# Optimization experiments

Measured on AMD Instinct MI355X. Metric: run time of the kernel, lower is better.

Reference implementation:

```python
import jax, jax.numpy as jnp
import numpy as np

B, N, IN_DIM, OUT_DIM = 8, 2048, 128, 64
TEMPERATURE = 1.0
NEG_SLOPE = 0.2


def setup_inputs() -> dict:
    key = jax.random.key(0)
    k1, k2, k3, k4, k5 = jax.random.split(key, 5)
    s_fc = 1.0 / np.sqrt(IN_DIM)
    s_at = 1.0 / np.sqrt(2 * OUT_DIM)
    return {
        "h": jax.random.normal(k1, (B, N, IN_DIM), dtype=jnp.float32),
        "W_fc": jax.random.normal(k2, (IN_DIM, OUT_DIM), dtype=jnp.float32) * s_fc,
        "b_fc": jax.random.normal(k3, (OUT_DIM,), dtype=jnp.float32) * s_fc,
        "a_src": jax.random.normal(k4, (OUT_DIM,), dtype=jnp.float32) * s_at,
        "a_dst": jax.random.normal(k5, (OUT_DIM,), dtype=jnp.float32) * s_at,
        "b_attn": jnp.zeros((), dtype=jnp.float32),
    }


def reference(h, W_fc, b_fc, a_src, a_dst, b_attn):
    # hp: (B, N, OUT_DIM) -- projected node features
    hp = h @ W_fc + b_fc
    # attn_fc(concat(h_i, h_j)) == h_i@a_src + h_j@a_dst + b (exact decomposition)
    s = hp @ a_src  # (B, N) source contribution
    d = hp @ a_dst  # (B, N) dest contribution
    scores = s[:, :, None] + d[:, None, :] + b_attn  # (B, N, N)
    scores = jnp.where(scores >= 0, scores, NEG_SLOPE * scores)  # leaky_relu
    scores = scores / TEMPERATURE
    attn = jax.nn.softmax(scores, axis=-1)
    out = jnp.einsum("bij,bjd->bid", attn, hp)
    return jax.nn.elu(out)
```

## Files before the change

### kernel.cpp

```cpp
#include <hip/hip_runtime.h>
#include <hip/hip_bf16.h>
#include <math.h>

#define BB 8
#define NN 2048
#define IND 128
#define OUTD 64
#define NEG 0.2f

typedef __attribute__((ext_vector_type(8))) short short8;
typedef __attribute__((ext_vector_type(4))) float f32x4;

__device__ __forceinline__ unsigned short f2bf(float f) {
    unsigned int u = __float_as_uint(f);
    u += 0x7fffu + ((u >> 16) & 1u);
    return (unsigned short)(u >> 16);
}

__device__ __forceinline__ unsigned int pk_bf16(float a, float b) {
    union { __hip_bfloat162 h; unsigned int u; } cv;
    cv.h = __float22bfloat162_rn(make_float2(a, b));
    return cv.u;
}

__global__ __launch_bounds__(256) void gat_proj_kernel(
    const float* __restrict__ h, const float* __restrict__ W,
    const float* __restrict__ bfc, const float* __restrict__ asrc,
    const float* __restrict__ adst,
    unsigned short* __restrict__ hpT2, float* __restrict__ s,
    float* __restrict__ F, float* __restrict__ H)
{
    __shared__ float Wl[IND * OUTD];
    __shared__ float hl[32 * 132];

    const int t  = threadIdx.x;
    const int R0 = blockIdx.x * 32;

    const float4* W4 = (const float4*)W;
    float4*       Wl4 = (float4*)Wl;
    #pragma unroll
    for (int k2 = 0; k2 < 8; ++k2) Wl4[t + k2 * 256] = W4[t + k2 * 256];

    const float4* h4 = (const float4*)(h + (size_t)R0 * IND);
    #pragma unroll
    for (int k2 = 0; k2 < 4; ++k2) {
        const int idx = t + k2 * 256;
        const int row = idx >> 5, c4 = idx & 31;
        *(float4*)&hl[row * 132 + c4 * 4] = h4[idx];
    }
    __syncthreads();

    const int r0 = (t >> 4) * 2;
    const int o0 = (t & 15) * 4;
    const float4 bias = *(const float4*)(bfc + o0);
    float4 a0 = bias, a1 = bias;

    #pragma unroll 2
    for (int kc = 0; kc < IND; kc += 4) {
        const float4 w0 = *(const float4*)&Wl[(kc + 0) * OUTD + o0];
        const float4 w1 = *(const float4*)&Wl[(kc + 1) * OUTD + o0];
        const float4 w2 = *(const float4*)&Wl[(kc + 2) * OUTD + o0];
        const float4 w3 = *(const float4*)&Wl[(kc + 3) * OUTD + o0];
        const float4 h0 = *(const float4*)&hl[(r0 + 0) * 132 + kc];
        const float4 h1 = *(const float4*)&hl[(r0 + 1) * 132 + kc];

        a0.x = fmaf(h0.x, w0.x, a0.x); a0.y = fmaf(h0.x, w0.y, a0.y);
        a0.z = fmaf(h0.x, w0.z, a0.z); a0.w = fmaf(h0.x, w0.w, a0.w);
        a0.x = fmaf(h0.y, w1.x, a0.x); a0.y = fmaf(h0.y, w1.y, a0.y);
        a0.z = fmaf(h0.y, w1.z, a0.z); a0.w = fmaf(h0.y, w1.w, a0.w);
        a0.x = fmaf(h0.z, w2.x, a0.x); a0.y = fmaf(h0.z, w2.y, a0.y);
        a0.z = fmaf(h0.z, w2.z, a0.z); a0.w = fmaf(h0.z, w2.w, a0.w);
        a0.x = fmaf(h0.w, w3.x, a0.x); a0.y = fmaf(h0.w, w3.y, a0.y);
        a0.z = fmaf(h0.w, w3.z, a0.z); a0.w = fmaf(h0.w, w3.w, a0.w);

        a1.x = fmaf(h1.x, w0.x, a1.x); a1.y = fmaf(h1.x, w0.y, a1.y);
        a1.z = fmaf(h1.x, w0.z, a1.z); a1.w = fmaf(h1.x, w0.w, a1.w);
        a1.x = fmaf(h1.y, w1.x, a1.x); a1.y = fmaf(h1.y, w1.y, a1.y);
        a1.z = fmaf(h1.y, w1.z, a1.z); a1.w = fmaf(h1.y, w1.w, a1.w);
        a1.x = fmaf(h1.z, w2.x, a1.x); a1.y = fmaf(h1.z, w2.y, a1.y);
        a1.z = fmaf(h1.z, w2.z, a1.z); a1.w = fmaf(h1.z, w2.w, a1.w);
        a1.x = fmaf(h1.w, w3.x, a1.x); a1.y = fmaf(h1.w, w3.y, a1.y);
        a1.z = fmaf(h1.w, w3.z, a1.z); a1.w = fmaf(h1.w, w3.w, a1.w);
    }

    const int b   = R0 >> 11;
    const int jb0 = (R0 & 2047) + r0;
    const int cj  = jb0 >> 3;
    const int sub = jb0 & 7;
    unsigned short* cbase = hpT2 + (((size_t)(b * 256 + cj)) * OUTD) * 8;
    {
        ushort2 v;
        v.x = f2bf(a0.x); v.y = f2bf(a1.x);
        *(ushort2*)(cbase + (o0 + 0) * 8 + sub) = v;
        v.x = f2bf(a0.y); v.y = f2bf(a1.y);
        *(ushort2*)(cbase + (o0 + 1) * 8 + sub) = v;
        v.x = f2bf(a0.z); v.y = f2bf(a1.z);
        *(ushort2*)(cbase + (o0 + 2) * 8 + sub) = v;
        v.x = f2bf(a0.w); v.y = f2bf(a1.w);
        *(ushort2*)(cbase + (o0 + 3) * 8 + sub) = v;
    }

    const float4 as4 = *(const float4*)(asrc + o0);
    const float4 ad4 = *(const float4*)(adst + o0);
    float vs[2], vd[2];
    vs[0] = a0.x*as4.x + a0.y*as4.y + a0.z*as4.z + a0.w*as4.w;
    vs[1] = a1.x*as4.x + a1.y*as4.y + a1.z*as4.z + a1.w*as4.w;
    vd[0] = a0.x*ad4.x + a0.y*ad4.y + a0.z*ad4.z + a0.w*ad4.w;
    vd[1] = a1.x*ad4.x + a1.y*ad4.y + a1.z*ad4.z + a1.w*ad4.w;
    #pragma unroll
    for (int msk = 1; msk <= 8; msk <<= 1) {
        vs[0] += __shfl_xor(vs[0], msk);
        vs[1] += __shfl_xor(vs[1], msk);
        vd[0] += __shfl_xor(vd[0], msk);
        vd[1] += __shfl_xor(vd[1], msk);
    }
    if ((t & 15) == 0) {
        #pragma unroll
        for (int r = 0; r < 2; ++r) {
            s[R0 + r0 + r] = vs[r];
            F[R0 + r0 + r] = __expf(vd[r]);
            H[R0 + r0 + r] = __expf(NEG * vd[r]);
        }
    }
}

__global__ __launch_bounds__(256) void gat_attn_kernel(
    const unsigned short* __restrict__ hpT2, const float* __restrict__ s,
    const float* __restrict__ F, const float* __restrict__ H,
    const float* __restrict__ battn_p, float* __restrict__ out)
{
    __shared__ float accl[4][64 * 66];
    __shared__ float ll[4][64];

    const int t    = threadIdx.x;
    const int lane = t & 63;
    const int wv   = t >> 6;
    const int blk  = blockIdx.x;
    const int b    = blk >> 5;
    const int i0   = (blk & 31) * 64;
    const int m    = lane & 15;
    const int kc   = lane >> 4;

    const float battn = battn_p[0];
    float E[4], G[4];
    #pragma unroll
    for (int T = 0; T < 4; ++T) {
        const float smv = s[b * NN + i0 + T * 16 + m] + battn;
        E[T] = __expf(smv);
        G[T] = __expf(NEG * smv);
    }
    const float* Fb = F + b * NN;
    const float* Hb = H + b * NN;
    const unsigned short* hb = hpT2 + (size_t)b * 256 * OUTD * 8;

    short8 ones;
    #pragma unroll
    for (int q = 0; q < 8; ++q) ones[q] = (short)0x3F80;

    f32x4 acc[4][4];
    f32x4 dacc[4];
    #pragma unroll
    for (int T = 0; T < 4; ++T) {
        dacc[T] = (f32x4){0.f, 0.f, 0.f, 0.f};
        #pragma unroll
        for (int ot = 0; ot < 4; ++ot) acc[T][ot] = (f32x4){0.f, 0.f, 0.f, 0.f};
    }

    const int jbase = wv * (NN / 4);

    #pragma unroll 2
    for (int it = 0; it < NN / 4 / 32; ++it) {
        const int j0 = jbase + it * 32;
        const size_t cb = ((size_t)((j0 >> 3) + kc)) * OUTD * 8;
        const short8 bf0 = *(const short8*)(hb + cb + (0 * 16 + m) * 8);
        const short8 bf1 = *(const short8*)(hb + cb + (1 * 16 + m) * 8);
        const short8 bf2 = *(const short8*)(hb + cb + (2 * 16 + m) * 8);
        const short8 bf3 = *(const short8*)(hb + cb + (3 * 16 + m) * 8);

        const float4 Fa = *(const float4*)(Fb + j0 + kc * 8);
        const float4 Fc = *(const float4*)(Fb + j0 + kc * 8 + 4);
        const float4 Ha = *(const float4*)(Hb + j0 + kc * 8);
        const float4 Hc = *(const float4*)(Hb + j0 + kc * 8 + 4);

        #pragma unroll
        for (int T = 0; T < 4; ++T) {
            const float Ei = E[T], Gi = G[T];
            float wf[8];
            wf[0] = fmaxf(Ei * Fa.x, Gi * Ha.x);
            wf[1] = fmaxf(Ei * Fa.y, Gi * Ha.y);
            wf[2] = fmaxf(Ei * Fa.z, Gi * Ha.z);
            wf[3] = fmaxf(Ei * Fa.w, Gi * Ha.w);
            wf[4] = fmaxf(Ei * Fc.x, Gi * Hc.x);
            wf[5] = fmaxf(Ei * Fc.y, Gi * Hc.y);
            wf[6] = fmaxf(Ei * Fc.z, Gi * Hc.z);
            wf[7] = fmaxf(Ei * Fc.w, Gi * Hc.w);

            union { short8 s8; unsigned int u[4]; } af;
            af.u[0] = pk_bf16(wf[0], wf[1]);
            af.u[1] = pk_bf16(wf[2], wf[3]);
            af.u[2] = pk_bf16(wf[4], wf[5]);
            af.u[3] = pk_bf16(wf[6], wf[7]);

            acc[T][0] = __builtin_amdgcn_mfma_f32_16x16x32_bf16(af.s8, bf0, acc[T][0], 0, 0, 0);
            acc[T][1] = __builtin_amdgcn_mfma_f32_16x16x32_bf16(af.s8, bf1, acc[T][1], 0, 0, 0);
            acc[T][2] = __builtin_amdgcn_mfma_f32_16x16x32_bf16(af.s8, bf2, acc[T][2], 0, 0, 0);
            acc[T][3] = __builtin_amdgcn_mfma_f32_16x16x32_bf16(af.s8, bf3, acc[T][3], 0, 0, 0);
            dacc[T]   = __builtin_amdgcn_mfma_f32_16x16x32_bf16(af.s8, ones, dacc[T], 0, 0, 0);
        }
    }

    if (m == 0) {
        #pragma unroll
        for (int T = 0; T < 4; ++T)
            #pragma unroll
            for (int r = 0; r < 4; ++r) ll[wv][T * 16 + kc * 4 + r] = dacc[T][r];
    }

    #pragma unroll
    for (int T = 0; T < 4; ++T) {
        #pragma unroll
        for (int r = 0; r < 4; ++r) {
            const int row = T * 16 + kc * 4 + r;
            accl[wv][row * 66 + 0 * 16 + m] = acc[T][0][r];
            accl[wv][row * 66 + 1 * 16 + m] = acc[T][1][r];
            accl[wv][row * 66 + 2 * 16 + m] = acc[T][2][r];
            accl[wv][row * 66 + 3 * 16 + m] = acc[T][3][r];
        }
    }
    __syncthreads();

    const int col = t & 63;
    const int r0e = (t >> 6) * 16;
    float* ob = out + (((size_t)b * NN + i0) * OUTD);
    #pragma unroll 4
    for (int r = 0; r < 16; ++r) {
        const int row = r0e + r;
        const float lsum = (ll[0][row] + ll[1][row]) + (ll[2][row] + ll[3][row]);
        float v = (accl[0][row * 66 + col] + accl[1][row * 66 + col]) +
                  (accl[2][row * 66 + col] + accl[3][row * 66 + col]);
        v /= lsum;
        v = (v > 0.f) ? v : expm1f(v);
        ob[(size_t)row * OUTD + col] = v;
    }
}

extern "C" void kernel_launch(void* const* d_in, const int* in_sizes, int n_in,
                              void* d_out, int out_size, void* d_ws, size_t ws_size,
                              hipStream_t stream)
{
    const float* h     = (const float*)d_in[0];
    const float* W     = (const float*)d_in[1];
    const float* bfc   = (const float*)d_in[2];
    const float* asrc  = (const float*)d_in[3];
    const float* adst  = (const float*)d_in[4];
    const float* battn = (const float*)d_in[5];
    float* out = (float*)d_out;

    unsigned short* hpT2 = (unsigned short*)d_ws;
    float* s = (float*)((char*)d_ws + (size_t)BB * NN * OUTD * 2);
    float* F = s + (size_t)BB * NN;
    float* H = F + (size_t)BB * NN;

    gat_proj_kernel<<<(BB * NN) / 32, 256, 0, stream>>>(h, W, bfc, asrc, adst,
                                                        hpT2, s, F, H);
    gat_attn_kernel<<<BB * (NN / 64), 256, 0, stream>>>(hpT2, s, F, H, battn, out);
}
```

Baseline: 91.17 us.

## Switch attention path to fp16 packed math and eight-wave blocks

Projected features and the exp factors F/H are stored as fp16 instead of bf16/fp32. Attention weights are built with packed half2 multiply/max instead of scalar fp32 ops plus bf16 conversion, and fed to f16 MFMA. Both kernels move to 512-thread blocks: the attention kernel splits the j range over eight waves and reduces partial accumulators through shared memory in two phases. This cuts VALU work and load bandwidth in the inner loop, at the cost of fp16 range risk for exp values and an extra sync in the reduction.

```diff
diff --git a/kernel.cpp b/kernel.cpp
--- a/kernel.cpp
+++ b/kernel.cpp
@@ -1,5 +1,4 @@
 #include <hip/hip_runtime.h>
-#include <hip/hip_bf16.h>
 #include <math.h>
 
 #define BB 8
@@ -8,43 +7,38 @@
 #define OUTD 64
 #define NEG 0.2f
 
-typedef __attribute__((ext_vector_type(8))) short short8;
 typedef __attribute__((ext_vector_type(4))) float f32x4;
-
-__device__ __forceinline__ unsigned short f2bf(float f) {
-    unsigned int u = __float_as_uint(f);
-    u += 0x7fffu + ((u >> 16) & 1u);
-    return (unsigned short)(u >> 16);
-}
-
-__device__ __forceinline__ unsigned int pk_bf16(float a, float b) {
-    union { __hip_bfloat162 h; unsigned int u; } cv;
-    cv.h = __float22bfloat162_rn(make_float2(a, b));
-    return cv.u;
-}
-
-__global__ __launch_bounds__(256) void gat_proj_kernel(
+typedef __attribute__((ext_vector_type(2))) _Float16 h2;
+typedef __attribute__((ext_vector_type(8))) _Float16 half8;
+
+__device__ __forceinline__ unsigned short f2h(float f) {
+    union { _Float16 h; unsigned short u; } c;
+    c.h = (_Float16)f;
+    return c.u;
+}
+
+__global__ __launch_bounds__(512) void gat_proj_kernel(
     const float* __restrict__ h, const float* __restrict__ W,
     const float* __restrict__ bfc, const float* __restrict__ asrc,
     const float* __restrict__ adst,
     unsigned short* __restrict__ hpT2, float* __restrict__ s,
-    float* __restrict__ F, float* __restrict__ H)
+    _Float16* __restrict__ F, _Float16* __restrict__ H)
 {
     __shared__ float Wl[IND * OUTD];
-    __shared__ float hl[32 * 132];
+    __shared__ float hl[64 * 132];
 
     const int t  = threadIdx.x;
-    const int R0 = blockIdx.x * 32;
+    const int R0 = blockIdx.x * 64;
 
     const float4* W4 = (const float4*)W;
     float4*       Wl4 = (float4*)Wl;
     #pragma unroll
-    for (int k2 = 0; k2 < 8; ++k2) Wl4[t + k2 * 256] = W4[t + k2 * 256];
+    for (int k2 = 0; k2 < 4; ++k2) Wl4[t + k2 * 512] = W4[t + k2 * 512];
 
     const float4* h4 = (const float4*)(h + (size_t)R0 * IND);
     #pragma unroll
     for (int k2 = 0; k2 < 4; ++k2) {
-        const int idx = t + k2 * 256;
+        const int idx = t + k2 * 512;
         const int row = idx >> 5, c4 = idx & 31;
         *(float4*)&hl[row * 132 + c4 * 4] = h4[idx];
     }
@@ -90,13 +84,13 @@
     unsigned short* cbase = hpT2 + (((size_t)(b * 256 + cj)) * OUTD) * 8;
     {
         ushort2 v;
-        v.x = f2bf(a0.x); v.y = f2bf(a1.x);
+        v.x = f2h(a0.x); v.y = f2h(a1.x);
         *(ushort2*)(cbase + (o0 + 0) * 8 + sub) = v;
-        v.x = f2bf(a0.y); v.y = f2bf(a1.y);
+        v.x = f2h(a0.y); v.y = f2h(a1.y);
         *(ushort2*)(cbase + (o0 + 1) * 8 + sub) = v;
-        v.x = f2bf(a0.z); v.y = f2bf(a1.z);
+        v.x = f2h(a0.z); v.y = f2h(a1.z);
         *(ushort2*)(cbase + (o0 + 2) * 8 + sub) = v;
-        v.x = f2bf(a0.w); v.y = f2bf(a1.w);
+        v.x = f2h(a0.w); v.y = f2h(a1.w);
         *(ushort2*)(cbase + (o0 + 3) * 8 + sub) = v;
     }
 
@@ -118,19 +112,19 @@
         #pragma unroll
         for (int r = 0; r < 2; ++r) {
             s[R0 + r0 + r] = vs[r];
-            F[R0 + r0 + r] = __expf(vd[r]);
-            H[R0 + r0 + r] = __expf(NEG * vd[r]);
-        }
-    }
-}
-
-__global__ __launch_bounds__(256) void gat_attn_kernel(
+            F[R0 + r0 + r] = (_Float16)__expf(vd[r]);
+            H[R0 + r0 + r] = (_Float16)__expf(NEG * vd[r]);
+        }
+    }
+}
+
+__global__ __launch_bounds__(512) void gat_attn_kernel(
     const unsigned short* __restrict__ hpT2, const float* __restrict__ s,
-    const float* __restrict__ F, const float* __restrict__ H,
+    const _Float16* __restrict__ F, const _Float16* __restrict__ H,
     const float* __restrict__ battn_p, float* __restrict__ out)
 {
     __shared__ float accl[4][64 * 66];
-    __shared__ float ll[4][64];
+    __shared__ float ll[8][64];
 
     const int t    = threadIdx.x;
     const int lane = t & 63;
@@ -142,20 +136,22 @@
     const int kc   = lane >> 4;
 
     const float battn = battn_p[0];
-    float E[4], G[4];
+    h2 E2[4], G2[4];
     #pragma unroll
     for (int T = 0; T < 4; ++T) {
         const float smv = s[b * NN + i0 + T * 16 + m] + battn;
-        E[T] = __expf(smv);
-        G[T] = __expf(NEG * smv);
-    }
-    const float* Fb = F + b * NN;
-    const float* Hb = H + b * NN;
-    const unsigned short* hb = hpT2 + (size_t)b * 256 * OUTD * 8;
-
-    short8 ones;
-    #pragma unroll
-    for (int q = 0; q < 8; ++q) ones[q] = (short)0x3F80;
+        const float Ef = __expf(smv);
+        const float Gf = __expf(NEG * smv);
+        E2[T] = (h2){(_Float16)Ef, (_Float16)Ef};
+        G2[T] = (h2){(_Float16)Gf, (_Float16)Gf};
+    }
+    const _Float16* Fb = F + b * NN;
+    const _Float16* Hb = H + b * NN;
+    const _Float16* hb = (const _Float16*)hpT2 + (size_t)b * 256 * OUTD * 8;
+
+    half8 ones;
+    #pragma unroll
+    for (int q = 0; q < 8; ++q) ones[q] = (_Float16)1.0f;
 
     f32x4 acc[4][4];
     f32x4 dacc[4];
@@ -166,46 +162,34 @@
         for (int ot = 0; ot < 4; ++ot) acc[T][ot] = (f32x4){0.f, 0.f, 0.f, 0.f};
     }
 
-    const int jbase = wv * (NN / 4);
+    const int jbase = wv * (NN / 8);
 
     #pragma unroll 2
-    for (int it = 0; it < NN / 4 / 32; ++it) {
+    for (int it = 0; it < NN / 8 / 32; ++it) {
         const int j0 = jbase + it * 32;
         const size_t cb = ((size_t)((j0 >> 3) + kc)) * OUTD * 8;
-        const short8 bf0 = *(const short8*)(hb + cb + (0 * 16 + m) * 8);
-        const short8 bf1 = *(const short8*)(hb + cb + (1 * 16 + m) * 8);
-        const short8 bf2 = *(const short8*)(hb + cb + (2 * 16 + m) * 8);
-        const short8 bf3 = *(const short8*)(hb + cb + (3 * 16 + m) * 8);
-
-        const float4 Fa = *(const float4*)(Fb + j0 + kc * 8);
-        const float4 Fc = *(const float4*)(Fb + j0 + kc * 8 + 4);
-        const float4 Ha = *(const float4*)(Hb + j0 + kc * 8);
-        const float4 Hc = *(const float4*)(Hb + j0 + kc * 8 + 4);
+        const half8 bf0 = *(const half8*)(hb + cb + (0 * 16 + m) * 8);
+        const half8 bf1 = *(const half8*)(hb + cb + (1 * 16 + m) * 8);
+        const half8 bf2 = *(const half8*)(hb + cb + (2 * 16 + m) * 8);
+        const half8 bf3 = *(const half8*)(hb + cb + (3 * 16 + m) * 8);
+
+        union { float4 q; h2 p[4]; } Ff, Hf;
+        Ff.q = *(const float4*)(Fb + j0 + kc * 8);
+        Hf.q = *(const float4*)(Hb + j0 + kc * 8);
 
         #pragma unroll
         for (int T = 0; T < 4; ++T) {
-            const float Ei = E[T], Gi = G[T];
-            float wf[8];
-            wf[0] = fmaxf(Ei * Fa.x, Gi * Ha.x);
-            wf[1] = fmaxf(Ei * Fa.y, Gi * Ha.y);
-            wf[2] = fmaxf(Ei * Fa.z, Gi * Ha.z);
-            wf[3] = fmaxf(Ei * Fa.w, Gi * Ha.w);
-            wf[4] = fmaxf(Ei * Fc.x, Gi * Hc.x);
-            wf[5] = fmaxf(Ei * Fc.y, Gi * Hc.y);
-            wf[6] = fmaxf(Ei * Fc.z, Gi * Hc.z);
-            wf[7] = fmaxf(Ei * Fc.w, Gi * Hc.w);
-
-            union { short8 s8; unsigned int u[4]; } af;
-            af.u[0] = pk_bf16(wf[0], wf[1]);
-            af.u[1] = pk_bf16(wf[2], wf[3]);
-            af.u[2] = pk_bf16(wf[4], wf[5]);
-            af.u[3] = pk_bf16(wf[6], wf[7]);
-
-            acc[T][0] = __builtin_amdgcn_mfma_f32_16x16x32_bf16(af.s8, bf0, acc[T][0], 0, 0, 0);
-            acc[T][1] = __builtin_amdgcn_mfma_f32_16x16x32_bf16(af.s8, bf1, acc[T][1], 0, 0, 0);
-            acc[T][2] = __builtin_amdgcn_mfma_f32_16x16x32_bf16(af.s8, bf2, acc[T][2], 0, 0, 0);
-            acc[T][3] = __builtin_amdgcn_mfma_f32_16x16x32_bf16(af.s8, bf3, acc[T][3], 0, 0, 0);
-            dacc[T]   = __builtin_amdgcn_mfma_f32_16x16x32_bf16(af.s8, ones, dacc[T], 0, 0, 0);
+            union { half8 v; h2 p[4]; } af;
+            af.p[0] = __builtin_elementwise_max(E2[T] * Ff.p[0], G2[T] * Hf.p[0]);
+            af.p[1] = __builtin_elementwise_max(E2[T] * Ff.p[1], G2[T] * Hf.p[1]);
+            af.p[2] = __builtin_elementwise_max(E2[T] * Ff.p[2], G2[T] * Hf.p[2]);
+            af.p[3] = __builtin_elementwise_max(E2[T] * Ff.p[3], G2[T] * Hf.p[3]);
+
+            acc[T][0] = __builtin_amdgcn_mfma_f32_16x16x32_f16(af.v, bf0, acc[T][0], 0, 0, 0);
+            acc[T][1] = __builtin_amdgcn_mfma_f32_16x16x32_f16(af.v, bf1, acc[T][1], 0, 0, 0);
+            acc[T][2] = __builtin_amdgcn_mfma_f32_16x16x32_f16(af.v, bf2, acc[T][2], 0, 0, 0);
+            acc[T][3] = __builtin_amdgcn_mfma_f32_16x16x32_f16(af.v, bf3, acc[T][3], 0, 0, 0);
+            dacc[T]   = __builtin_amdgcn_mfma_f32_16x16x32_f16(af.v, ones, dacc[T], 0, 0, 0);
         }
     }
 
@@ -216,26 +200,43 @@
             for (int r = 0; r < 4; ++r) ll[wv][T * 16 + kc * 4 + r] = dacc[T][r];
     }
 
-    #pragma unroll
-    for (int T = 0; T < 4; ++T) {
-        #pragma unroll
-        for (int r = 0; r < 4; ++r) {
-            const int row = T * 16 + kc * 4 + r;
-            accl[wv][row * 66 + 0 * 16 + m] = acc[T][0][r];
-            accl[wv][row * 66 + 1 * 16 + m] = acc[T][1][r];
-            accl[wv][row * 66 + 2 * 16 + m] = acc[T][2][r];
-            accl[wv][row * 66 + 3 * 16 + m] = acc[T][3][r];
+    if (wv >= 4) {
+        #pragma unroll
+        for (int T = 0; T < 4; ++T) {
+            #pragma unroll
+            for (int r = 0; r < 4; ++r) {
+                const int row = T * 16 + kc * 4 + r;
+                accl[wv - 4][row * 66 + 0 * 16 + m] = acc[T][0][r];
+                accl[wv - 4][row * 66 + 1 * 16 + m] = acc[T][1][r];
+                accl[wv - 4][row * 66 + 2 * 16 + m] = acc[T][2][r];
+                accl[wv - 4][row * 66 + 3 * 16 + m] = acc[T][3][r];
+            }
         }
     }
     __syncthreads();
+    if (wv < 4) {
+        #pragma unroll
+        for (int T = 0; T < 4; ++T) {
+            #pragma unroll
+            for (int r = 0; r < 4; ++r) {
+                const int row = T * 16 + kc * 4 + r;
+                accl[wv][row * 66 + 0 * 16 + m] += acc[T][0][r];
+                accl[wv][row * 66 + 1 * 16 + m] += acc[T][1][r];
+                accl[wv][row * 66 + 2 * 16 + m] += acc[T][2][r];
+                accl[wv][row * 66 + 3 * 16 + m] += acc[T][3][r];
+            }
+        }
+    }
+    __syncthreads();
 
     const int col = t & 63;
-    const int r0e = (t >> 6) * 16;
+    const int r0e = (t >> 6) * 8;
     float* ob = out + (((size_t)b * NN + i0) * OUTD);
     #pragma unroll 4
-    for (int r = 0; r < 16; ++r) {
+    for (int r = 0; r < 8; ++r) {
         const int row = r0e + r;
-        const float lsum = (ll[0][row] + ll[1][row]) + (ll[2][row] + ll[3][row]);
+        const float lsum = ((ll[0][row] + ll[1][row]) + (ll[2][row] + ll[3][row])) +
+                           ((ll[4][row] + ll[5][row]) + (ll[6][row] + ll[7][row]));
         float v = (accl[0][row * 66 + col] + accl[1][row * 66 + col]) +
                   (accl[2][row * 66 + col] + accl[3][row * 66 + col]);
         v /= lsum;
@@ -257,11 +258,11 @@
     float* out = (float*)d_out;
 
     unsigned short* hpT2 = (unsigned short*)d_ws;
-    float* s = (float*)((char*)d_ws + (size_t)BB * NN * OUTD * 2);
-    float* F = s + (size_t)BB * NN;
-    float* H = F + (size_t)BB * NN;
-
-    gat_proj_kernel<<<(BB * NN) / 32, 256, 0, stream>>>(h, W, bfc, asrc, adst,
+    float*     s = (float*)((char*)d_ws + (size_t)BB * NN * OUTD * 2);
+    _Float16*  F = (_Float16*)(s + (size_t)BB * NN);
+    _Float16*  H = F + (size_t)BB * NN;
+
+    gat_proj_kernel<<<(BB * NN) / 64, 512, 0, stream>>>(h, W, bfc, asrc, adst,
                                                         hpT2, s, F, H);
-    gat_attn_kernel<<<BB * (NN / 64), 256, 0, stream>>>(hpT2, s, F, H, battn, out);
-}
+    gat_attn_kernel<<<BB * (NN / 64), 512, 0, stream>>>(hpT2, s, F, H, battn, out);
+}
```

New measurement: 83.98 us. -7.9%, faster.
